# Optimization experiments

Hardware: AMD Instinct MI355X
Metric: run time of the kernel (lower is better)

The kernel has to match this reference:

```python
import jax, jax.numpy as jnp
import numpy as np

DELTA_VAR = 0.1
DELTA_DIST = 0.3
ALPHA = 1.0
BETA = 1.0
C = 2048  # number of superpixels (static; torch derives it as sp_seg.max()+1)


def setup_inputs() -> dict:
    key = jax.random.key(0)
    k1, k2, k3, k4 = jax.random.split(key, 4)
    B, E, H, W = 4, 32, 512, 512
    n_edges = 8192
    embeddings = jax.random.normal(k1, (B, E, H, W), dtype=jnp.float32)
    sp_seg = jax.random.randint(k2, (B, 1, H, W), 0, C)
    edges = jax.random.randint(k3, (B, 2, n_edges), 0, C)
    weights = jax.random.uniform(k4, (B, n_edges), dtype=jnp.float32)
    return {"embeddings": embeddings, "sp_seg": sp_seg, "edges": edges, "weights": weights}


def _per_sample(emb, seg, edg, w):
    # emb: [E,H,W], seg: [1,H,W], edg: [2,n_edges], w: [n_edges]
    E = emb.shape[0]
    N = emb.shape[1] * emb.shape[2]
    emb_f = emb.reshape(E, N).T              # [N,E]
    seg_f = seg.reshape(N)                   # [N]
    counts = jax.ops.segment_sum(jnp.ones((N,), emb.dtype), seg_f, num_segments=C)  # [C]
    sums = jax.ops.segment_sum(emb_f, seg_f, num_segments=C)                         # [C,E]
    means = sums / jnp.maximum(counts, 1.0)[:, None]
    norm = jnp.sqrt(jnp.sum(means * means, axis=-1, keepdims=True))
    means = means / jnp.maximum(norm, 1e-10)  # L2-normalized superpixel means [C,E]
    # intra-superpixel distance: 1 - <mean_sp(pix), emb(pix)> per pixel
    d = 1.0 - jnp.sum(means[seg_f] * emb_f, axis=-1)  # [N]
    intra = jnp.sum(jnp.maximum(d - DELTA_VAR, 0.0) / counts[seg_f]) / C
    # inter-superpixel distance along RAG edges
    f0 = means[edg[0]]                       # [n_edges,E]
    f1 = means[edg[1]]
    inter = 1.0 - jnp.sum(f0 * f1, axis=-1)  # [n_edges]
    inter = jnp.maximum(DELTA_DIST - inter * w, 0.0)
    inter = jnp.sum(inter) / edg.shape[1]
    return ALPHA * inter + BETA * intra


def reference(embeddings, sp_seg, edges, weights):
    per_sample = jax.vmap(_per_sample)(embeddings, sp_seg, edges, weights)  # [B]
    return jnp.sum(per_sample)  # scalar (torch sums over batch then .mean() of a 1-elem tensor)
```

## Files before the change

### kernel.cpp

```cpp
#include <hip/hip_runtime.h>

#define BN 4
#define EN 32
#define NPIX (512 * 512)
#define CSEG 2048
#define NEDGE 8192

#define DELTA_VAR 0.1f
#define DELTA_DIST 0.3f

#define FP_SCALE 262144.0f
#define FP_INV (1.0 / 262144.0)
#define FP_BIAS 16.0f

typedef unsigned long long u64;


__global__ __launch_bounds__(512) void rag_accum(
    const float* __restrict__ emb, const int* __restrict__ seg,
    unsigned int* __restrict__ counts, u64* __restrict__ sums64) {
  __shared__ u64 lsum[4 * CSEG];
  __shared__ unsigned int lcnt[CSEG];

  const int pb = blockIdx.x & 31;
  const int fam = (blockIdx.x >> 5) & 3;
  const int b = blockIdx.x >> 7;

  for (int i = threadIdx.x; i < 4 * CSEG; i += 512) lsum[i] = 0ull;
  if (fam == 0)
    for (int i = threadIdx.x; i < CSEG; i += 512) lcnt[i] = 0u;
  __syncthreads();

  const int ppb = NPIX / 32;
  const int p0 = pb * ppb;
  const float* __restrict__ eb = emb + ((size_t)b * EN + fam * 8) * NPIX;
  const int* __restrict__ sb = seg + (size_t)b * NPIX;

  for (int p = p0 + threadIdx.x; p < p0 + ppb; p += 512) {
    const int s = sb[p];
    if (fam == 0) atomicAdd(&lcnt[s], 1u);
#pragma unroll
    for (int pr = 0; pr < 4; pr++) {
      const float v0 = eb[(size_t)(2 * pr) * NPIX + p];
      const float v1 = eb[(size_t)(2 * pr + 1) * NPIX + p];
      const unsigned int q0 = (unsigned int)__float2int_rn((v0 + FP_BIAS) * FP_SCALE);
      const unsigned int q1 = (unsigned int)__float2int_rn((v1 + FP_BIAS) * FP_SCALE);
      atomicAdd(&lsum[pr * CSEG + s], ((u64)q1 << 32) | (u64)q0);
    }
  }
  __syncthreads();

  for (int i = threadIdx.x; i < 4 * CSEG; i += 512) {
    const int pr = i >> 11;
    const int c = i & (CSEG - 1);
    atomicAdd(&sums64[((size_t)(fam * 4 + pr) * BN + b) * CSEG + c], lsum[i]);
  }
  if (fam == 0) {
    for (int i = threadIdx.x; i < CSEG; i += 512) {
      const unsigned int v = lcnt[i];
      if (v) atomicAdd(&counts[b * CSEG + i], v);
    }
  }
}

__global__ __launch_bounds__(256) void rag_finalize(
    const unsigned int* __restrict__ counts, const u64* __restrict__ sums64,
    float* __restrict__ means) {
  const int idx = blockIdx.x * 256 + threadIdx.x;
  if (idx >= BN * CSEG) return;
  const int b = idx >> 11;
  const int c = idx & (CSEG - 1);
  const int cnt = (int)counts[idx];
  const double bias = 16.0 * (double)cnt;
  const double inv = 1.0 / (double)(cnt > 1 ? cnt : 1);
  float m[EN];
  double nrm = 0.0;
#pragma unroll
  for (int k = 0; k < 16; k++) {
    const u64 sq = sums64[((size_t)k * BN + b) * CSEG + c];
    const double s0 = (double)(unsigned int)(sq & 0xffffffffull) * FP_INV - bias;
    const double s1 = (double)(unsigned int)(sq >> 32) * FP_INV - bias;
    const double m0 = s0 * inv, m1 = s1 * inv;
    m[2 * k] = (float)m0;
    m[2 * k + 1] = (float)m1;
    nrm += m0 * m0 + m1 * m1;
  }
  const float sc = (float)(1.0 / fmax(sqrt(nrm), 1e-10));
  float* __restrict__ mb = means + (size_t)idx * EN;
#pragma unroll
  for (int e = 0; e < EN; e++) mb[e] = m[e] * sc;
}

__global__ __launch_bounds__(256) void rag_intra(
    const float* __restrict__ emb, const int* __restrict__ seg,
    const unsigned int* __restrict__ counts, const float* __restrict__ means,
    float* __restrict__ out) {
  const int t = blockIdx.x * 256 + threadIdx.x;
  const int b = t >> 16;
  const int p4 = (t & 65535) << 2;
  const int4 s4 = *(const int4*)(seg + (size_t)b * NPIX + p4);
  const float* __restrict__ eb = emb + (size_t)b * EN * NPIX + p4;
  const float* __restrict__ mb = means + (size_t)b * CSEG * EN;
  const float* __restrict__ m0 = mb + (size_t)s4.x * EN;
  const float* __restrict__ m1 = mb + (size_t)s4.y * EN;
  const float* __restrict__ m2 = mb + (size_t)s4.z * EN;
  const float* __restrict__ m3 = mb + (size_t)s4.w * EN;
  float d0 = 0.f, d1 = 0.f, d2 = 0.f, d3 = 0.f;
#pragma unroll
  for (int e = 0; e < EN; e++) {
    const float4 v = *(const float4*)(eb + (size_t)e * NPIX);
    d0 += m0[e] * v.x;
    d1 += m1[e] * v.y;
    d2 += m2[e] * v.z;
    d3 += m3[e] * v.w;
  }
  const unsigned int* __restrict__ cb = counts + b * CSEG;
  float acc = 0.f;
  {
    const float u0 = 1.0f - d0 - DELTA_VAR;
    const float u1 = 1.0f - d1 - DELTA_VAR;
    const float u2 = 1.0f - d2 - DELTA_VAR;
    const float u3 = 1.0f - d3 - DELTA_VAR;
    if (u0 > 0.f) acc += u0 / (float)cb[s4.x];
    if (u1 > 0.f) acc += u1 / (float)cb[s4.y];
    if (u2 > 0.f) acc += u2 / (float)cb[s4.z];
    if (u3 > 0.f) acc += u3 / (float)cb[s4.w];
  }
  for (int o = 32; o > 0; o >>= 1) acc += __shfl_down(acc, o, 64);
  __shared__ float wsum[4];
  const int lane = threadIdx.x & 63;
  const int wid = threadIdx.x >> 6;
  if (lane == 0) wsum[wid] = acc;
  __syncthreads();
  if (threadIdx.x == 0) {
    atomicAdd(out, (wsum[0] + wsum[1] + wsum[2] + wsum[3]) * (1.0f / CSEG));
  }
}

#define JTHREADS 256
__global__ __launch_bounds__(JTHREADS) void rag_inter(
    const int* __restrict__ edges, const float* __restrict__ weights,
    const float* __restrict__ means, float* __restrict__ out) {
  const int idx = blockIdx.x * JTHREADS + threadIdx.x;
  float val = 0.0f;
  if (idx < BN * NEDGE) {
    const int b = idx >> 13;
    const int k = idx & (NEDGE - 1);
    const int e0 = edges[(size_t)b * 2 * NEDGE + k];
    const int e1 = edges[(size_t)b * 2 * NEDGE + NEDGE + k];
    const float w = weights[idx];
    const float4* __restrict__ ma =
        (const float4*)(means + ((size_t)b * CSEG + e0) * EN);
    const float4* __restrict__ mc =
        (const float4*)(means + ((size_t)b * CSEG + e1) * EN);
    float dot = 0.0f;
#pragma unroll
    for (int e4 = 0; e4 < EN / 4; e4++) {
      const float4 a = ma[e4];
      const float4 c = mc[e4];
      dot += a.x * c.x + a.y * c.y + a.z * c.z + a.w * c.w;
    }
    val = fmaxf(DELTA_DIST - (1.0f - dot) * w, 0.0f);
  }
  for (int o = 32; o > 0; o >>= 1) val += __shfl_down(val, o, 64);
  __shared__ float wsum[JTHREADS / 64];
  const int lane = threadIdx.x & 63;
  const int wid = threadIdx.x >> 6;
  if (lane == 0) wsum[wid] = val;
  __syncthreads();
  if (threadIdx.x == 0) {
    float bsum = 0.0f;
#pragma unroll
    for (int w = 0; w < JTHREADS / 64; w++) bsum += wsum[w];
    atomicAdd(out, bsum * (1.0f / NEDGE));
  }
}

extern "C" void kernel_launch(void* const* d_in, const int* in_sizes, int n_in,
                              void* d_out, int out_size, void* d_ws, size_t ws_size,
                              hipStream_t stream) {
  const float* emb = (const float*)d_in[0];
  const int* seg = (const int*)d_in[1];
  const int* edges = (const int*)d_in[2];
  const float* weights = (const float*)d_in[3];
  float* out = (float*)d_out;

  unsigned int* counts = (unsigned int*)d_ws;
  u64* sums64 = (u64*)((char*)d_ws + (size_t)BN * CSEG * 4);
  float* means = (float*)(sums64 + (size_t)16 * BN * CSEG);

  hipMemsetAsync(d_out, 0, (size_t)out_size * sizeof(float), stream);
  hipMemsetAsync(d_ws, 0, (size_t)BN * CSEG * 4 + (size_t)16 * BN * CSEG * 8,
                 stream);

  rag_accum<<<512, 512, 0, stream>>>(emb, seg, counts, sums64);
  rag_finalize<<<(BN * CSEG + 255) / 256, 256, 0, stream>>>(counts, sums64, means);
  rag_intra<<<BN * NPIX / 4 / 256, 256, 0, stream>>>(emb, seg, counts, means, out);
  rag_inter<<<(BN * NEDGE + JTHREADS - 1) / JTHREADS, JTHREADS, 0, stream>>>(
      edges, weights, means, out);
}
```

Baseline: 103.4 us.

## Pack three 21-bit fixed-point embedding sums per 64-bit atomic

Lowers the fixed-point scale and packs three quantized channels into each 64-bit LDS atomic instead of two. This cuts the number of shared and global atomics per pixel, and the work is regrouped into six block families, with counts handled by the last family. The trade is coarser quantization of the superpixel sums (step 1/256), which may reduce the accuracy of the means.

```diff
diff --git a/kernel.cpp b/kernel.cpp
--- a/kernel.cpp
+++ b/kernel.cpp
@@ -9,9 +9,11 @@
 #define DELTA_VAR 0.1f
 #define DELTA_DIST 0.3f
 
-#define FP_SCALE 262144.0f
-#define FP_INV (1.0 / 262144.0)
+#define FP_SCALE 256.0f
+#define FP_INV (1.0 / 256.0)
 #define FP_BIAS 16.0f
+#define NGRP 11
+#define MASK21 ((1ull << 21) - 1)
 
 typedef unsigned long long u64;
 
@@ -19,44 +21,71 @@
 __global__ __launch_bounds__(512) void rag_accum(
     const float* __restrict__ emb, const int* __restrict__ seg,
     unsigned int* __restrict__ counts, u64* __restrict__ sums64) {
-  __shared__ u64 lsum[4 * CSEG];
+  __shared__ u64 lsum[2 * CSEG];
   __shared__ unsigned int lcnt[CSEG];
 
-  const int pb = blockIdx.x & 31;
-  const int fam = (blockIdx.x >> 5) & 3;
-  const int b = blockIdx.x >> 7;
-
-  for (int i = threadIdx.x; i < 4 * CSEG; i += 512) lsum[i] = 0ull;
-  if (fam == 0)
+  const int blk = blockIdx.x;
+  const int pb = blk & 31;
+  const int t = blk >> 5;
+  const int fam = t % 6;
+  const int b = t / 6;
+
+  for (int i = threadIdx.x; i < 2 * CSEG; i += 512) lsum[i] = 0ull;
+  if (fam == 5)
     for (int i = threadIdx.x; i < CSEG; i += 512) lcnt[i] = 0u;
   __syncthreads();
 
   const int ppb = NPIX / 32;
   const int p0 = pb * ppb;
-  const float* __restrict__ eb = emb + ((size_t)b * EN + fam * 8) * NPIX;
   const int* __restrict__ sb = seg + (size_t)b * NPIX;
 
-  for (int p = p0 + threadIdx.x; p < p0 + ppb; p += 512) {
-    const int s = sb[p];
-    if (fam == 0) atomicAdd(&lcnt[s], 1u);
-#pragma unroll
-    for (int pr = 0; pr < 4; pr++) {
-      const float v0 = eb[(size_t)(2 * pr) * NPIX + p];
-      const float v1 = eb[(size_t)(2 * pr + 1) * NPIX + p];
-      const unsigned int q0 = (unsigned int)__float2int_rn((v0 + FP_BIAS) * FP_SCALE);
-      const unsigned int q1 = (unsigned int)__float2int_rn((v1 + FP_BIAS) * FP_SCALE);
-      atomicAdd(&lsum[pr * CSEG + s], ((u64)q1 << 32) | (u64)q0);
-    }
-  }
-  __syncthreads();
-
-  for (int i = threadIdx.x; i < 4 * CSEG; i += 512) {
-    const int pr = i >> 11;
-    const int c = i & (CSEG - 1);
-    atomicAdd(&sums64[((size_t)(fam * 4 + pr) * BN + b) * CSEG + c], lsum[i]);
-  }
-  if (fam == 0) {
+  if (fam < 5) {
+    const float* __restrict__ eb = emb + ((size_t)b * EN + 6 * fam) * NPIX;
+    for (int p = p0 + threadIdx.x; p < p0 + ppb; p += 512) {
+      const int s = sb[p];
+      u64 pk0, pk1;
+      {
+        const unsigned int q0 =
+            (unsigned int)__float2int_rn((eb[p] + FP_BIAS) * FP_SCALE);
+        const unsigned int q1 =
+            (unsigned int)__float2int_rn((eb[p + NPIX] + FP_BIAS) * FP_SCALE);
+        const unsigned int q2 =
+            (unsigned int)__float2int_rn((eb[p + 2 * NPIX] + FP_BIAS) * FP_SCALE);
+        pk0 = (u64)q0 | ((u64)q1 << 21) | ((u64)q2 << 42);
+      }
+      {
+        const unsigned int q3 =
+            (unsigned int)__float2int_rn((eb[p + 3 * NPIX] + FP_BIAS) * FP_SCALE);
+        const unsigned int q4 =
+            (unsigned int)__float2int_rn((eb[p + 4 * NPIX] + FP_BIAS) * FP_SCALE);
+        const unsigned int q5 =
+            (unsigned int)__float2int_rn((eb[p + 5 * NPIX] + FP_BIAS) * FP_SCALE);
+        pk1 = (u64)q3 | ((u64)q4 << 21) | ((u64)q5 << 42);
+      }
+      atomicAdd(&lsum[s], pk0);
+      atomicAdd(&lsum[CSEG + s], pk1);
+    }
+    __syncthreads();
+    const int g0 = 2 * fam;
+    for (int i = threadIdx.x; i < 2 * CSEG; i += 512) {
+      const int g = g0 + (i >> 11);
+      const int c = i & (CSEG - 1);
+      atomicAdd(&sums64[((size_t)g * BN + b) * CSEG + c], lsum[i]);
+    }
+  } else {
+    const float* __restrict__ eb = emb + ((size_t)b * EN + 30) * NPIX;
+    for (int p = p0 + threadIdx.x; p < p0 + ppb; p += 512) {
+      const int s = sb[p];
+      const unsigned int q0 =
+          (unsigned int)__float2int_rn((eb[p] + FP_BIAS) * FP_SCALE);
+      const unsigned int q1 =
+          (unsigned int)__float2int_rn((eb[p + NPIX] + FP_BIAS) * FP_SCALE);
+      atomicAdd(&lsum[s], (u64)q0 | ((u64)q1 << 21));
+      atomicAdd(&lcnt[s], 1u);
+    }
+    __syncthreads();
     for (int i = threadIdx.x; i < CSEG; i += 512) {
+      atomicAdd(&sums64[((size_t)10 * BN + b) * CSEG + i], lsum[i]);
       const unsigned int v = lcnt[i];
       if (v) atomicAdd(&counts[b * CSEG + i], v);
     }
@@ -71,18 +100,29 @@
   const int b = idx >> 11;
   const int c = idx & (CSEG - 1);
   const int cnt = (int)counts[idx];
-  const double bias = 16.0 * (double)cnt;
+  const double bias = (double)FP_BIAS * (double)cnt;
   const double inv = 1.0 / (double)(cnt > 1 ? cnt : 1);
   float m[EN];
   double nrm = 0.0;
 #pragma unroll
-  for (int k = 0; k < 16; k++) {
-    const u64 sq = sums64[((size_t)k * BN + b) * CSEG + c];
-    const double s0 = (double)(unsigned int)(sq & 0xffffffffull) * FP_INV - bias;
-    const double s1 = (double)(unsigned int)(sq >> 32) * FP_INV - bias;
+  for (int g = 0; g < 10; g++) {
+    const u64 sq = sums64[((size_t)g * BN + b) * CSEG + c];
+    const double s0 = (double)(sq & MASK21) * FP_INV - bias;
+    const double s1 = (double)((sq >> 21) & MASK21) * FP_INV - bias;
+    const double s2 = (double)(sq >> 42) * FP_INV - bias;
+    const double m0 = s0 * inv, m1 = s1 * inv, m2 = s2 * inv;
+    m[3 * g] = (float)m0;
+    m[3 * g + 1] = (float)m1;
+    m[3 * g + 2] = (float)m2;
+    nrm += m0 * m0 + m1 * m1 + m2 * m2;
+  }
+  {
+    const u64 sq = sums64[((size_t)10 * BN + b) * CSEG + c];
+    const double s0 = (double)(sq & MASK21) * FP_INV - bias;
+    const double s1 = (double)((sq >> 21) & MASK21) * FP_INV - bias;
     const double m0 = s0 * inv, m1 = s1 * inv;
-    m[2 * k] = (float)m0;
-    m[2 * k + 1] = (float)m1;
+    m[30] = (float)m0;
+    m[31] = (float)m1;
     nrm += m0 * m0 + m1 * m1;
   }
   const float sc = (float)(1.0 / fmax(sqrt(nrm), 1e-10));
@@ -187,13 +227,13 @@
 
   unsigned int* counts = (unsigned int*)d_ws;
   u64* sums64 = (u64*)((char*)d_ws + (size_t)BN * CSEG * 4);
-  float* means = (float*)(sums64 + (size_t)16 * BN * CSEG);
+  float* means = (float*)(sums64 + (size_t)NGRP * BN * CSEG);
 
   hipMemsetAsync(d_out, 0, (size_t)out_size * sizeof(float), stream);
-  hipMemsetAsync(d_ws, 0, (size_t)BN * CSEG * 4 + (size_t)16 * BN * CSEG * 8,
-                 stream);
-
-  rag_accum<<<512, 512, 0, stream>>>(emb, seg, counts, sums64);
+  hipMemsetAsync(d_ws, 0,
+                 (size_t)BN * CSEG * 4 + (size_t)NGRP * BN * CSEG * 8, stream);
+
+  rag_accum<<<32 * 6 * BN, 512, 0, stream>>>(emb, seg, counts, sums64);
   rag_finalize<<<(BN * CSEG + 255) / 256, 256, 0, stream>>>(counts, sums64, means);
   rag_intra<<<BN * NPIX / 4 / 256, 256, 0, stream>>>(emb, seg, counts, means, out);
   rag_inter<<<(BN * NEDGE + JTHREADS - 1) / JTHREADS, JTHREADS, 0, stream>>>(
```

Result: faster. 88.11 us (-14.8%).
